# Performance work log

Hardware: AMD Instinct MI355X
Metric: run time of the kernel (lower is better)

## Reference

```python
import jax, jax.numpy as jnp
import numpy as np

NUM_EXPERTS = 128
TOP_K = 4
HIDDEN = 2880
T = 8192


def setup_inputs() -> dict:
    key = jax.random.key(0)
    kx, kw = jax.random.split(key)
    x = jax.random.normal(kx, (T, HIDDEN), dtype=jnp.float32)
    weight = jax.random.normal(kw, (NUM_EXPERTS, HIDDEN), dtype=jnp.float32) * 0.02
    bias = jnp.zeros((NUM_EXPERTS,), dtype=jnp.float32)
    return {"x": x, "weight": weight, "bias": bias}


def reference(x, weight, bias):
    # logits: (T, E) = x @ W^T + b
    logits = jnp.einsum("th,eh->te", x, weight) + bias
    # top-k logits per token (softmax AFTER topk, matching HF semantics)
    top_logits, top_indices = jax.lax.top_k(logits, TOP_K)  # (T, K)
    top_scores = jax.nn.softmax(top_logits, axis=-1)
    # histogram of expert assignments == bincount over flattened indices
    flat = top_indices.reshape(-1)
    num_tokens_per_expert = jax.ops.segment_sum(
        jnp.ones_like(flat, dtype=jnp.float32), flat, num_segments=NUM_EXPERTS
    )
    return top_scores, top_indices, num_tokens_per_expert
```

## Files before the change

kernel.cpp:

```cpp
#include <hip/hip_runtime.h>
#include <math.h>

#define T_TOK 8192
#define HID   2880
#define NE    128
#define TOPK  4
#define NKS   (HID / 32)
#define TM    64
#define SPLITK 4
#define LROW  40
#define LPLANE (TM * LROW)

typedef _Float16 f16x8 __attribute__((ext_vector_type(8)));
typedef _Float16 f16x4 __attribute__((ext_vector_type(4)));
typedef float    f32x4 __attribute__((ext_vector_type(4)));

__global__ __launch_bounds__(256) void convert_w(const float* __restrict__ w,
                                                 _Float16* __restrict__ wc) {
  const int c = blockIdx.x * 256 + threadIdx.x;
  if (c >= NE * (HID / 8)) return;
  const int n  = c / (HID / 8);
  const int k8 = c % (HID / 8);
  const float4 v0 = *(const float4*)(w + (size_t)n * HID + k8 * 8);
  const float4 v1 = *(const float4*)(w + (size_t)n * HID + k8 * 8 + 4);
  const float f[8] = {v0.x, v0.y, v0.z, v0.w, v1.x, v1.y, v1.z, v1.w};
  f16x8 h, l;
#pragma unroll
  for (int i = 0; i < 8; ++i) {
    const float s = f[i] * 32.0f;
    const _Float16 hi = (_Float16)s;
    h[i] = hi;
    l[i] = (_Float16)(s - (float)hi);
  }
  const int gs   = k8 >> 2;
  const int oct  = k8 & 3;
  const int j    = n >> 4;
  const int lane = (oct << 4) | (n & 15);
  _Float16* base = wc + ((size_t)(gs * 8 + j) * 2) * 512 + lane * 8;
  *(f16x8*)(base)       = h;
  *(f16x8*)(base + 512) = l;
}

struct BF { f16x8 h[2], l[2]; };

__device__ __forceinline__ void load_b(const _Float16* __restrict__ wc, int wn,
                                       int lane, int gs, BF& f) {
#pragma unroll
  for (int g = 0; g < 2; ++g) {
    const _Float16* bp = wc + ((size_t)(gs * 8 + wn * 2 + g) * 2) * 512 + lane * 8;
    f.h[g] = *(const f16x8*)bp;
    f.l[g] = *(const f16x8*)(bp + 512);
  }
}

__device__ __forceinline__ void load_x(const float* __restrict__ x, int m0,
                                       int t, int gs, float4 (&xr)[2]) {
#pragma unroll
  for (int j = 0; j < 2; ++j) {
    const int c   = j * 256 + t;
    const int row = c >> 3;
    const int kq  = c & 7;
    xr[j] = *(const float4*)(x + (size_t)(m0 + row) * HID + gs * 32 + kq * 4);
  }
}

__device__ __forceinline__ void stage_x(const float4 (&xr)[2],
                                        _Float16* __restrict__ buf, int t) {
#pragma unroll
  for (int j = 0; j < 2; ++j) {
    const int c   = j * 256 + t;
    const int row = c >> 3;
    const int kq  = c & 7;
    const float a[4] = {xr[j].x, xr[j].y, xr[j].z, xr[j].w};
    f16x4 h, l;
#pragma unroll
    for (int i = 0; i < 4; ++i) {
      const _Float16 hi = (_Float16)a[i];
      h[i] = hi;
      l[i] = (_Float16)(a[i] - (float)hi);
    }
    const int off = row * LROW + kq * 4;
    *(f16x4*)&buf[off]          = h;
    *(f16x4*)&buf[LPLANE + off] = l;
  }
}

__device__ __forceinline__ void mfma_step(const _Float16* __restrict__ buf,
                                          const BF& f, int lane,
                                          f32x4 (&acc)[4][2]) {
#pragma unroll
  for (int mi = 0; mi < 4; ++mi) {
    const int off = (mi * 16 + (lane & 15)) * LROW + (lane >> 4) * 8;
    const f16x8 ah = *(const f16x8*)&buf[off];
    const f16x8 al = *(const f16x8*)&buf[LPLANE + off];
#pragma unroll
    for (int g = 0; g < 2; ++g) {
      acc[mi][g] = __builtin_amdgcn_mfma_f32_16x16x32_f16(ah, f.h[g], acc[mi][g], 0, 0, 0);
      acc[mi][g] = __builtin_amdgcn_mfma_f32_16x16x32_f16(al, f.h[g], acc[mi][g], 0, 0, 0);
      acc[mi][g] = __builtin_amdgcn_mfma_f32_16x16x32_f16(ah, f.l[g], acc[mi][g], 0, 0, 0);
    }
  }
}

__global__ __launch_bounds__(256, 2) void logits_mfma(const float* __restrict__ x,
                                                      const _Float16* __restrict__ wc,
                                                      float* __restrict__ part) {
  __shared__ _Float16 xsh[2 * 2 * LPLANE];

  const int bid = blockIdx.x;
  const int s    = bid & 3;
  const int tile = ((bid >> 3) << 1) | ((bid & 7) >> 2);
  const int m0   = tile * TM;

  const int t    = threadIdx.x;
  const int lane = t & 63;
  const int wn   = t >> 6;

  const int kbase = NKS / SPLITK, krem = NKS % SPLITK;
  const int cnt   = kbase + (s < krem ? 1 : 0);
  const int st0   = s * kbase + (s < krem ? s : krem);

  _Float16* buf0 = xsh;
  _Float16* buf1 = xsh + 2 * LPLANE;

  f32x4 acc[4][2] = {};
  float4 xrA[2], xrB[2];
  BF bA, bB;

  load_x(x, m0, t, st0, xrA);
  load_b(wc, wn, lane, st0, bA);
  stage_x(xrA, buf0, t);
  if (cnt > 1) load_x(x, m0, t, st0 + 1, xrB);
  __syncthreads();

  int st = 0;
  for (;;) {
    if (st + 1 < cnt) load_b(wc, wn, lane, st0 + st + 1, bB);
    if (st + 2 < cnt) load_x(x, m0, t, st0 + st + 2, xrA);
    mfma_step(buf0, bA, lane, acc);
    if (st + 1 < cnt) stage_x(xrB, buf1, t);
    __syncthreads();
    if (st + 1 >= cnt) break;

    if (st + 2 < cnt) load_b(wc, wn, lane, st0 + st + 2, bA);
    if (st + 3 < cnt) load_x(x, m0, t, st0 + st + 3, xrB);
    mfma_step(buf1, bB, lane, acc);
    if (st + 2 < cnt) stage_x(xrA, buf0, t);
    __syncthreads();
    st += 2;
    if (st >= cnt) break;
  }

  float* pl = part + (size_t)s * T_TOK * NE;
  const int e0 = wn * 32 + (lane & 15);
  const int r0 = m0 + (lane >> 4) * 4;
#pragma unroll
  for (int mi = 0; mi < 4; ++mi)
#pragma unroll
    for (int g = 0; g < 2; ++g) {
      float* pp = pl + (size_t)(r0 + mi * 16) * NE + e0 + g * 16;
#pragma unroll
      for (int r = 0; r < 4; ++r) pp[(size_t)r * NE] = acc[mi][g][r] * 0.03125f;
    }
}

__global__ __launch_bounds__(256) void topk_kernel(const float* __restrict__ part,
                                                   const float* __restrict__ bias,
                                                   float* __restrict__ out) {
  const int lane = threadIdx.x & 63;
  const int wave = threadIdx.x >> 6;
  const int tok  = blockIdx.x * 4 + wave;

  float v0 = 0.f, v1 = 0.f;
#pragma unroll
  for (int s = 0; s < SPLITK; ++s) {
    const float2 p = ((const float2*)(part + ((size_t)s * T_TOK + tok) * NE))[lane];
    v0 += p.x;
    v1 += p.y;
  }
  const float2 b2 = ((const float2*)bias)[lane];
  v0 += b2.x;
  v1 += b2.y;
  const int i0 = 2 * lane, i1 = 2 * lane + 1;

  float topv[TOPK];
  int   topi[TOPK];

#pragma unroll
  for (int r = 0; r < TOPK; ++r) {
    float bv; int bi;
    if (v0 >= v1) { bv = v0; bi = i0; }
    else          { bv = v1; bi = i1; }
#pragma unroll
    for (int off = 32; off > 0; off >>= 1) {
      const float ov = __shfl_xor(bv, off);
      const int   oi = __shfl_xor(bi, off);
      if (ov > bv || (ov == bv && oi < bi)) { bv = ov; bi = oi; }
    }
    topv[r] = bv; topi[r] = bi;
    if (bi == i0) v0 = -INFINITY;
    if (bi == i1) v1 = -INFINITY;
  }

  const float m = topv[0];
  float sum = 0.f;
#pragma unroll
  for (int r = 0; r < TOPK; ++r) sum += expf(topv[r] - m);

  if (lane < TOPK) {
    out[(size_t)tok * TOPK + lane] = expf(topv[lane] - m) / sum;
    out[(size_t)T_TOK * TOPK + (size_t)tok * TOPK + lane] = (float)topi[lane];
  }
}

__global__ __launch_bounds__(256) void count_kernel(const float* __restrict__ idxf,
                                                    float* __restrict__ counts) {
  const int e = blockIdx.x;
  const int t = threadIdx.x;
  const float ef = (float)e;
  int c = 0;
  for (int i = t; i < T_TOK * TOPK; i += 256)
    c += (idxf[i] == ef) ? 1 : 0;
#pragma unroll
  for (int off = 32; off > 0; off >>= 1) c += __shfl_xor(c, off);
  __shared__ int shred[4];
  if ((t & 63) == 0) shred[t >> 6] = c;
  __syncthreads();
  if (t == 0) counts[e] = (float)(shred[0] + shred[1] + shred[2] + shred[3]);
}

extern "C" void kernel_launch(void* const* d_in, const int* in_sizes, int n_in,
                              void* d_out, int out_size, void* d_ws, size_t ws_size,
                              hipStream_t stream) {
  const float* x    = (const float*)d_in[0];
  const float* w    = (const float*)d_in[1];
  const float* bias = (const float*)d_in[2];
  float* out  = (float*)d_out;
  float* part = (float*)d_ws;
  _Float16* wc = (_Float16*)((char*)d_ws +
                             (size_t)SPLITK * T_TOK * NE * sizeof(float));

  convert_w<<<(NE * (HID / 8) + 255) / 256, 256, 0, stream>>>(w, wc);
  logits_mfma<<<(T_TOK / TM) * SPLITK, 256, 0, stream>>>(x, wc, part);
  topk_kernel<<<T_TOK / 4, 256, 0, stream>>>(part, bias, out);
  count_kernel<<<NE, 256, 0, stream>>>(out + (size_t)T_TOK * TOPK,
                                       out + 2 * (size_t)T_TOK * TOPK);
}
```

Measured before the change: 60.70 us.

## Fuse top-k into GEMM via last-split-block reduction and per-tile histograms

Each split-K GEMM block bumps an atomic counter for its tile after writing its partials. The last block to finish reduces the four partials, applies bias, and runs top-k and softmax for the tile's 64 tokens. It also builds a shared-memory expert histogram, which a single small kernel then sums across tiles. This removes the separate top-k launch and the 128-block count kernel that rescanned all indices. The cost is atomics, thread fences, and a serialized tail in which only one block per tile does the top-k work.

```diff
diff --git a/kernel.cpp b/kernel.cpp
--- a/kernel.cpp
+++ b/kernel.cpp
@@ -7,6 +7,7 @@
 #define TOPK  4
 #define NKS   (HID / 32)
 #define TM    64
+#define NTILE (T_TOK / TM)
 #define SPLITK 4
 #define LROW  40
 #define LPLANE (TM * LROW)
@@ -16,7 +17,9 @@
 typedef float    f32x4 __attribute__((ext_vector_type(4)));
 
 __global__ __launch_bounds__(256) void convert_w(const float* __restrict__ w,
-                                                 _Float16* __restrict__ wc) {
+                                                 _Float16* __restrict__ wc,
+                                                 int* __restrict__ ctr) {
+  if (blockIdx.x == 0 && threadIdx.x < NTILE) ctr[threadIdx.x] = 0;
   const int c = blockIdx.x * 256 + threadIdx.x;
   if (c >= NE * (HID / 8)) return;
   const int n  = c / (HID / 8);
@@ -102,10 +105,16 @@
   }
 }
 
-__global__ __launch_bounds__(256, 2) void logits_mfma(const float* __restrict__ x,
-                                                      const _Float16* __restrict__ wc,
-                                                      float* __restrict__ part) {
+__global__ __launch_bounds__(256, 2) void gemm_topk(const float* __restrict__ x,
+                                                    const _Float16* __restrict__ wc,
+                                                    const float* __restrict__ bias,
+                                                    float* __restrict__ part,
+                                                    int* __restrict__ ctr,
+                                                    float* __restrict__ tileHist,
+                                                    float* __restrict__ out) {
   __shared__ _Float16 xsh[2 * 2 * LPLANE];
+  __shared__ int hist[NE];
+  __shared__ int lastFlag;
 
   const int bid = blockIdx.x;
   const int s    = bid & 3;
@@ -162,71 +171,71 @@
 #pragma unroll
       for (int r = 0; r < 4; ++r) pp[(size_t)r * NE] = acc[mi][g][r] * 0.03125f;
     }
-}
-
-__global__ __launch_bounds__(256) void topk_kernel(const float* __restrict__ part,
-                                                   const float* __restrict__ bias,
-                                                   float* __restrict__ out) {
-  const int lane = threadIdx.x & 63;
-  const int wave = threadIdx.x >> 6;
-  const int tok  = blockIdx.x * 4 + wave;
-
-  float v0 = 0.f, v1 = 0.f;
-#pragma unroll
-  for (int s = 0; s < SPLITK; ++s) {
-    const float2 p = ((const float2*)(part + ((size_t)s * T_TOK + tok) * NE))[lane];
-    v0 += p.x;
-    v1 += p.y;
-  }
-  const float2 b2 = ((const float2*)bias)[lane];
-  v0 += b2.x;
-  v1 += b2.y;
-  const int i0 = 2 * lane, i1 = 2 * lane + 1;
-
-  float topv[TOPK];
-  int   topi[TOPK];
-
-#pragma unroll
-  for (int r = 0; r < TOPK; ++r) {
-    float bv; int bi;
-    if (v0 >= v1) { bv = v0; bi = i0; }
-    else          { bv = v1; bi = i1; }
-#pragma unroll
-    for (int off = 32; off > 0; off >>= 1) {
-      const float ov = __shfl_xor(bv, off);
-      const int   oi = __shfl_xor(bi, off);
-      if (ov > bv || (ov == bv && oi < bi)) { bv = ov; bi = oi; }
-    }
-    topv[r] = bv; topi[r] = bi;
-    if (bi == i0) v0 = -INFINITY;
-    if (bi == i1) v1 = -INFINITY;
-  }
-
-  const float m = topv[0];
-  float sum = 0.f;
-#pragma unroll
-  for (int r = 0; r < TOPK; ++r) sum += expf(topv[r] - m);
-
-  if (lane < TOPK) {
-    out[(size_t)tok * TOPK + lane] = expf(topv[lane] - m) / sum;
-    out[(size_t)T_TOK * TOPK + (size_t)tok * TOPK + lane] = (float)topi[lane];
-  }
-}
-
-__global__ __launch_bounds__(256) void count_kernel(const float* __restrict__ idxf,
+
+  __threadfence();
+  __syncthreads();
+  if (t == 0) lastFlag = (atomicAdd(&ctr[tile], 1) == SPLITK - 1);
+  __syncthreads();
+  if (!lastFlag) return;
+  __threadfence();
+
+  for (int e = t; e < NE; e += 256) hist[e] = 0;
+  __syncthreads();
+
+  for (int i = 0; i < 16; ++i) {
+    const int tok = m0 + wn * 16 + i;
+    float v0 = 0.f, v1 = 0.f;
+#pragma unroll
+    for (int sp = 0; sp < SPLITK; ++sp) {
+      const float2 p = ((const float2*)(part + ((size_t)sp * T_TOK + tok) * NE))[lane];
+      v0 += p.x;
+      v1 += p.y;
+    }
+    const float2 b2 = ((const float2*)bias)[lane];
+    v0 += b2.x;
+    v1 += b2.y;
+    const int i0 = 2 * lane, i1 = 2 * lane + 1;
+
+    float topv[TOPK];
+    int   topi[TOPK];
+#pragma unroll
+    for (int r = 0; r < TOPK; ++r) {
+      float bv; int bi;
+      if (v0 >= v1) { bv = v0; bi = i0; }
+      else          { bv = v1; bi = i1; }
+#pragma unroll
+      for (int off = 32; off > 0; off >>= 1) {
+        const float ov = __shfl_xor(bv, off);
+        const int   oi = __shfl_xor(bi, off);
+        if (ov > bv || (ov == bv && oi < bi)) { bv = ov; bi = oi; }
+      }
+      topv[r] = bv; topi[r] = bi;
+      if (bi == i0) v0 = -INFINITY;
+      if (bi == i1) v1 = -INFINITY;
+    }
+
+    const float m = topv[0];
+    float sum = 0.f;
+#pragma unroll
+    for (int r = 0; r < TOPK; ++r) sum += expf(topv[r] - m);
+
+    if (lane < TOPK) {
+      out[(size_t)tok * TOPK + lane] = expf(topv[lane] - m) / sum;
+      out[(size_t)T_TOK * TOPK + (size_t)tok * TOPK + lane] = (float)topi[lane];
+      atomicAdd(&hist[topi[lane]], 1);
+    }
+  }
+  __syncthreads();
+  for (int e = t; e < NE; e += 256)
+    tileHist[(size_t)tile * NE + e] = (float)hist[e];
+}
+
+__global__ __launch_bounds__(128) void count_reduce(const float* __restrict__ tileHist,
                                                     float* __restrict__ counts) {
-  const int e = blockIdx.x;
-  const int t = threadIdx.x;
-  const float ef = (float)e;
-  int c = 0;
-  for (int i = t; i < T_TOK * TOPK; i += 256)
-    c += (idxf[i] == ef) ? 1 : 0;
-#pragma unroll
-  for (int off = 32; off > 0; off >>= 1) c += __shfl_xor(c, off);
-  __shared__ int shred[4];
-  if ((t & 63) == 0) shred[t >> 6] = c;
-  __syncthreads();
-  if (t == 0) counts[e] = (float)(shred[0] + shred[1] + shred[2] + shred[3]);
+  const int e = threadIdx.x;
+  float c = 0.f;
+  for (int tl = 0; tl < NTILE; ++tl) c += tileHist[(size_t)tl * NE + e];
+  counts[e] = c;
 }
 
 extern "C" void kernel_launch(void* const* d_in, const int* in_sizes, int n_in,
@@ -235,14 +244,19 @@
   const float* x    = (const float*)d_in[0];
   const float* w    = (const float*)d_in[1];
   const float* bias = (const float*)d_in[2];
-  float* out  = (float*)d_out;
-  float* part = (float*)d_ws;
-  _Float16* wc = (_Float16*)((char*)d_ws +
-                             (size_t)SPLITK * T_TOK * NE * sizeof(float));
-
-  convert_w<<<(NE * (HID / 8) + 255) / 256, 256, 0, stream>>>(w, wc);
-  logits_mfma<<<(T_TOK / TM) * SPLITK, 256, 0, stream>>>(x, wc, part);
-  topk_kernel<<<T_TOK / 4, 256, 0, stream>>>(part, bias, out);
-  count_kernel<<<NE, 256, 0, stream>>>(out + (size_t)T_TOK * TOPK,
-                                       out + 2 * (size_t)T_TOK * TOPK);
-}
+  float* out = (float*)d_out;
+
+  char* ws = (char*)d_ws;
+  float*    part     = (float*)ws;
+  size_t    off      = (size_t)SPLITK * T_TOK * NE * sizeof(float);
+  _Float16* wc       = (_Float16*)(ws + off);
+  off += (size_t)NE * HID * 2 * sizeof(_Float16);
+  int*      ctr      = (int*)(ws + off);
+  off += NTILE * sizeof(int);
+  float*    tileHist = (float*)(ws + off);
+
+  convert_w<<<(NE * (HID / 8) + 255) / 256, 256, 0, stream>>>(w, wc, ctr);
+  gemm_topk<<<(T_TOK / TM) * SPLITK, 256, 0, stream>>>(x, wc, bias, part, ctr,
+                                                       tileHist, out);
+  count_reduce<<<1, 128, 0, stream>>>(tileHist, out + 2 * (size_t)T_TOK * TOPK);
+}
```

Result: slower. 157.9 us (+160.1%).
